# Kernel optimization log

Hardware: AMD Instinct MI355X
Metric: run time of the kernel (lower is better)

## Reference

```python
import jax, jax.numpy as jnp
import numpy as np

EMB, HEADS = 1024, 16
HS = EMB // HEADS
LN_EPS = 1e-5


def _layernorm(v, g, b):
    # normalize over last dim (headsize)
    mu = jnp.mean(v, axis=-1, keepdims=True)
    var = jnp.mean(jnp.square(v - mu), axis=-1, keepdims=True)
    return (v - mu) * jax.lax.rsqrt(var + LN_EPS) * g + b


def setup_inputs() -> dict:
    key = jax.random.key(0)
    ks = jax.random.split(key, 12)
    s = 1.0 / np.sqrt(EMB)
    return {
        "x": jax.random.normal(ks[0], (4, 2048, EMB), dtype=jnp.float32),
        "mask": jax.random.randint(ks[1], (4, 2048), 0, 2, dtype=jnp.int32),
        "Wk": jax.random.uniform(ks[2], (EMB, EMB), jnp.float32, -s, s),
        "Wq": jax.random.uniform(ks[3], (EMB, EMB), jnp.float32, -s, s),
        "Wv": jax.random.uniform(ks[4], (EMB, EMB), jnp.float32, -s, s),
        "Wo": jax.random.uniform(ks[5], (EMB, EMB), jnp.float32, -s, s),
        "bo": jax.random.uniform(ks[6], (EMB,), jnp.float32, -s, s),
        "kln_g": jnp.ones((HS,), jnp.float32),
        "kln_b": jnp.zeros((HS,), jnp.float32),
        "qln_g": jnp.ones((HS,), jnp.float32),
        "qln_b": jnp.zeros((HS,), jnp.float32),
    }


def reference(x, mask, Wk, Wq, Wv, Wo, bo, kln_g, kln_b, qln_g, qln_b):
    b, t, e = x.shape
    # QKV projections (torch Linear: y = x @ W.T), split into heads
    k = (x @ Wk.T).reshape(b, t, HEADS, HS)
    q = (x @ Wq.T).reshape(b, t, HEADS, HS)
    v = (x @ Wv.T).reshape(b, t, HEADS, HS)
    # per-head LayerNorm on K and Q
    k = _layernorm(k, kln_g, kln_b)
    q = _layernorm(q, qln_g, qln_b)
    # scale by emb^(1/4) on each side
    scale = jnp.asarray(e, x.dtype) ** 0.25
    q = q / scale
    k = k / scale
    # [b, h, tq, tk] attention logits
    dot = jnp.einsum("bqhd,bkhd->bhqk", q, k)
    # outer-product mask, broadcast over heads
    m = mask.astype(x.dtype)
    dm = m[:, None, :, None] * m[:, None, None, :]  # [b,1,tq,tk]
    # non-memory-efficient masked softmax: softmax(v*m)*m renormalized
    attn = jax.nn.softmax(dot * dm, axis=-1) * dm
    attn = attn / (jnp.sum(attn, axis=-1, keepdims=True) + 1e-13)
    out = jnp.einsum("bhqk,bkhd->bqhd", attn, v).reshape(b, t, e)
    return out @ Wo.T + bo
```

## Files before the change

kernel.cpp:

```cpp
#include <hip/hip_runtime.h>
#include <math.h>

#define B_SZ   4
#define T_SEQ  2048
#define EMB    1024
#define HEADS  16
#define HS     64
#define M_TOT  (B_SZ * T_SEQ)

typedef unsigned short u16;
using f32x4  = __attribute__((ext_vector_type(4))) float;
using bf16x8 = __attribute__((ext_vector_type(8))) short;
using u16x8  = __attribute__((ext_vector_type(8))) unsigned short;
using u16x4  = __attribute__((ext_vector_type(4))) unsigned short;

__device__ __forceinline__ void async16(u16* lds, const u16* g) {
    __builtin_amdgcn_global_load_lds(
        (const __attribute__((address_space(1))) unsigned int*)g,
        (__attribute__((address_space(3))) unsigned int*)lds, 16, 0, 0);
}

__device__ __forceinline__ u16 bf16_rne(float f) {
    unsigned u = __float_as_uint(f);
    return (u16)((u + 0x7fffu + ((u >> 16) & 1u)) >> 16);
}
__device__ __forceinline__ void split2(float f, u16& h, u16& l) {
    h = bf16_rne(f);
    float hf = __uint_as_float(((unsigned)h) << 16);
    l = bf16_rne(f - hf);
}
__device__ __forceinline__ unsigned cvt_pk_bf16(float a, float b) {
    unsigned r;
    asm("v_cvt_pk_bf16_f32 %0, %1, %2" : "=v"(r) : "v"(a), "v"(b));
    return r;
}

__global__ __launch_bounds__(256) void split_bf16(
    const float* __restrict__ in, u16* __restrict__ hi,
    u16* __restrict__ lo, int n4)
{
    int i = blockIdx.x * blockDim.x + threadIdx.x;
    if (i >= n4) return;
    float4 v = ((const float4*)in)[i];
    float f[4] = {v.x, v.y, v.z, v.w};
    u16 hh[4], ll[4];
    #pragma unroll
    for (int j = 0; j < 4; ++j) split2(f[j], hh[j], ll[j]);
    uint2 H, L;
    H.x = (unsigned)hh[0] | ((unsigned)hh[1] << 16);
    H.y = (unsigned)hh[2] | ((unsigned)hh[3] << 16);
    L.x = (unsigned)ll[0] | ((unsigned)ll[1] << 16);
    L.y = (unsigned)ll[2] | ((unsigned)ll[3] << 16);
    ((uint2*)hi)[i] = H;
    ((uint2*)lo)[i] = L;
}

#define BM 128
#define BN 128
#define BKB 32

__global__ __launch_bounds__(256, 2) void gemm_mfma(
    const u16* __restrict__ Ah, const u16* __restrict__ Al,
    const u16* __restrict__ Wh, const u16* __restrict__ Wl,
    float* __restrict__ Cf, u16* __restrict__ Chi, u16* __restrict__ Clo,
    const float* __restrict__ lng, const float* __restrict__ lnb,
    float post_scale, const float* __restrict__ bias, int mode)
{
    __shared__ u16 sAh[BM * BKB], sAl[BM * BKB];
    __shared__ u16 sBh[BN * BKB], sBl[BN * BKB];
    const int tid = threadIdx.x;
    const int w = tid >> 6, lane = tid & 63;
    const int wr = w >> 1, wc = w & 1;
    const int m0 = blockIdx.x * BM, n0 = blockIdx.y * BN;
    const int fr = lane & 15, kc = (lane >> 4) * 8;
    const int srow = lane >> 2, schunk = (lane & 3) * 8;

    f32x4 acc[4][4] = {};

    for (int k0 = 0; k0 < EMB; k0 += BKB) {
        #pragma unroll
        for (int c = 0; c < 2; ++c) {
            int r = (w * 2 + c) * 16 + srow;
            size_t gA = (size_t)(m0 + r) * EMB + k0 + schunk;
            size_t gB = (size_t)(n0 + r) * EMB + k0 + schunk;
            int lb = (w * 2 + c) * 512;
            async16(&sAh[lb], Ah + gA);
            async16(&sAl[lb], Al + gA);
            async16(&sBh[lb], Wh + gB);
            async16(&sBl[lb], Wl + gB);
        }
        __syncthreads();

        bf16x8 bh[4], bl[4];
        #pragma unroll
        for (int ni = 0; ni < 4; ++ni) {
            int row = wc * 64 + ni * 16 + fr;
            bh[ni] = *(const bf16x8*)&sBh[row * BKB + kc];
            bl[ni] = *(const bf16x8*)&sBl[row * BKB + kc];
        }
        #pragma unroll
        for (int mi = 0; mi < 4; ++mi) {
            int row = wr * 64 + mi * 16 + fr;
            bf16x8 ah = *(const bf16x8*)&sAh[row * BKB + kc];
            bf16x8 al = *(const bf16x8*)&sAl[row * BKB + kc];
            #pragma unroll
            for (int ni = 0; ni < 4; ++ni) {
                acc[mi][ni] = __builtin_amdgcn_mfma_f32_16x16x32_bf16(ah, bh[ni], acc[mi][ni], 0, 0, 0);
                acc[mi][ni] = __builtin_amdgcn_mfma_f32_16x16x32_bf16(ah, bl[ni], acc[mi][ni], 0, 0, 0);
                acc[mi][ni] = __builtin_amdgcn_mfma_f32_16x16x32_bf16(al, bh[ni], acc[mi][ni], 0, 0, 0);
            }
        }
        __syncthreads();
    }

    if (mode == 1) {
        float g4[4], b4[4];
        #pragma unroll
        for (int ni = 0; ni < 4; ++ni) {
            int dd = ni * 16 + fr;
            g4[ni] = lng[dd];
            b4[ni] = lnb[dd];
        }
        #pragma unroll
        for (int mi = 0; mi < 4; ++mi) {
            #pragma unroll
            for (int i = 0; i < 4; ++i) {
                float s = acc[mi][0][i] + acc[mi][1][i] + acc[mi][2][i] + acc[mi][3][i];
                #pragma unroll
                for (int off = 1; off < 16; off <<= 1) s += __shfl_xor(s, off);
                float mu = s * (1.f / HS);
                float d2 = 0.f;
                #pragma unroll
                for (int ni = 0; ni < 4; ++ni) {
                    float d = acc[mi][ni][i] - mu;
                    d2 += d * d;
                }
                #pragma unroll
                for (int off = 1; off < 16; off <<= 1) d2 += __shfl_xor(d2, off);
                float rs = rsqrtf(d2 * (1.f / HS) + 1e-5f);
                #pragma unroll
                for (int ni = 0; ni < 4; ++ni)
                    acc[mi][ni][i] = ((acc[mi][ni][i] - mu) * rs * g4[ni] + b4[ni]) * post_scale;
            }
        }
    }

    #pragma unroll
    for (int mi = 0; mi < 4; ++mi) {
        #pragma unroll
        for (int ni = 0; ni < 4; ++ni) {
            const int col = n0 + wc * 64 + ni * 16 + fr;
            const int rowb = m0 + wr * 64 + mi * 16 + (lane >> 4) * 4;
            if (mode == 0) {
                float badd = bias[col];
                #pragma unroll
                for (int i = 0; i < 4; ++i)
                    Cf[(size_t)(rowb + i) * EMB + col] = acc[mi][ni][i] + badd;
            } else if (mode == 1) {
                #pragma unroll
                for (int i = 0; i < 4; ++i) {
                    u16 hh, ll; split2(acc[mi][ni][i], hh, ll);
                    Chi[(size_t)(rowb + i) * EMB + col] = hh;
                    Clo[(size_t)(rowb + i) * EMB + col] = ll;
                }
            } else {
                int hh = col >> 6, d = col & 63;
                int bb = rowb >> 11, t0 = rowb & 2047;
                u16x4 H, L;
                #pragma unroll
                for (int i = 0; i < 4; ++i) {
                    u16 vh, vl; split2(acc[mi][ni][i], vh, vl);
                    H[i] = vh; L[i] = vl;
                }
                size_t off = ((size_t)((bb * HEADS + hh) * HS + d)) * T_SEQ + t0;
                *(u16x4*)(Chi + off) = H;
                *(u16x4*)(Clo + off) = L;
            }
        }
    }
}

__global__ __launch_bounds__(256, 2) void attn_mfma(
    const u16* __restrict__ qh, const u16* __restrict__ ql,
    const u16* __restrict__ kh, const u16* __restrict__ kl,
    const u16* __restrict__ vh, const u16* __restrict__ vl,
    const int* __restrict__ mask,
    u16* __restrict__ oh, u16* __restrict__ ol)
{
    __shared__ u16 sKh[64 * 72], sKl[64 * 72], sVh[64 * 72], sVl[64 * 72];
    __shared__ u16 sPs[4][32 * 72];
    __shared__ float kmsh[64];
    __shared__ float qmsh[128];
    __shared__ float fb[4][32];

    const int tid = threadIdx.x;
    const int w = tid >> 6, lane = tid & 63;
    const int fr = lane & 15, g = lane >> 4;
    const int q0 = blockIdx.x * 128;
    const int h = blockIdx.y, b = blockIdx.z;

    if (tid < 128) qmsh[tid] = (float)mask[b * T_SEQ + q0 + tid];

    const u16* ksrc; u16* sdst; size_t rstr, kstp;
    if (w < 2) {
        ksrc = (w == 0 ? kh : kl) + (size_t)b * T_SEQ * EMB + h * HS;
        sdst = (w == 0 ? sKh : sKl);
        rstr = EMB; kstp = (size_t)64 * EMB;
    } else {
        ksrc = (w == 2 ? vh : vl) + (size_t)(b * HEADS + h) * HS * T_SEQ;
        sdst = (w == 2 ? sVh : sVl);
        rstr = T_SEQ; kstp = 64;
    }

    bf16x8 qfh[2][2], qfl[2][2];
    #pragma unroll
    for (int nf = 0; nf < 2; ++nf)
        #pragma unroll
        for (int ks = 0; ks < 2; ++ks) {
            size_t off = (size_t)(b * T_SEQ + q0 + w * 32 + nf * 16 + fr) * EMB
                         + h * HS + g * 8 + ks * 32;
            qfh[nf][ks] = *(const bf16x8*)(qh + off);
            qfl[nf][ks] = *(const bf16x8*)(ql + off);
        }

    f32x4 o[2][4] = {};
    float mrun[2] = {-INFINITY, -INFINITY}, lrun[2] = {0.f, 0.f};
    u16* Psw = sPs[w];

    for (int kt = 0; kt < T_SEQ / 64; ++kt) {
        const u16* src = ksrc + (size_t)kt * kstp;
        u16x8 stg[8];
        #pragma unroll
        for (int it = 0; it < 8; ++it) {
            int idx = it * 64 + lane;
            stg[it] = *(const u16x8*)(src + (size_t)(idx >> 3) * rstr + (idx & 7) * 8);
        }
        #pragma unroll
        for (int it = 0; it < 8; ++it) {
            int idx = it * 64 + lane;
            *(u16x8*)&sdst[(idx >> 3) * 72 + (idx & 7) * 8] = stg[it];
        }
        if (tid < 64) kmsh[tid] = (float)mask[b * T_SEQ + kt * 64 + tid];
        __syncthreads();

        float kmv[4][4]; int anyv = 0;
        #pragma unroll
        for (int mf = 0; mf < 4; ++mf)
            #pragma unroll
            for (int i = 0; i < 4; ++i) {
                kmv[mf][i] = kmsh[mf * 16 + g * 4 + i];
                anyv |= (kmv[mf][i] != 0.f);
            }

        if (__any(anyv)) {
            f32x4 st[4][2] = {};
            #pragma unroll
            for (int ks = 0; ks < 2; ++ks) {
                bf16x8 ka[4], kb[4];
                #pragma unroll
                for (int mf = 0; mf < 4; ++mf) {
                    ka[mf] = *(const bf16x8*)&sKh[(mf * 16 + fr) * 72 + g * 8 + ks * 32];
                    kb[mf] = *(const bf16x8*)&sKl[(mf * 16 + fr) * 72 + g * 8 + ks * 32];
                }
                #pragma unroll
                for (int mf = 0; mf < 4; ++mf)
                    #pragma unroll
                    for (int nf = 0; nf < 2; ++nf) {
                        st[mf][nf] = __builtin_amdgcn_mfma_f32_16x16x32_bf16(ka[mf], qfh[nf][ks], st[mf][nf], 0, 0, 0);
                        st[mf][nf] = __builtin_amdgcn_mfma_f32_16x16x32_bf16(ka[mf], qfl[nf][ks], st[mf][nf], 0, 0, 0);
                        st[mf][nf] = __builtin_amdgcn_mfma_f32_16x16x32_bf16(kb[mf], qfh[nf][ks], st[mf][nf], 0, 0, 0);
                    }
            }
            #pragma unroll
            for (int nf = 0; nf < 2; ++nf) {
                float tm = -INFINITY;
                #pragma unroll
                for (int mf = 0; mf < 4; ++mf)
                    #pragma unroll
                    for (int i = 0; i < 4; ++i) {
                        float s = (kmv[mf][i] != 0.f) ? st[mf][nf][i] : -INFINITY;
                        st[mf][nf][i] = s;
                        tm = fmaxf(tm, s);
                    }
                tm = fmaxf(tm, __shfl_xor(tm, 16));
                tm = fmaxf(tm, __shfl_xor(tm, 32));
                float mn = fmaxf(mrun[nf], tm);
                float f = __expf(mrun[nf] - mn);
                float ps = 0.f;
                #pragma unroll
                for (int mf = 0; mf < 4; ++mf)
                    #pragma unroll
                    for (int i = 0; i < 4; ++i) {
                        float p = __expf(st[mf][nf][i] - mn);
                        st[mf][nf][i] = p;
                        ps += p;
                    }
                ps += __shfl_xor(ps, 16);
                ps += __shfl_xor(ps, 32);
                lrun[nf] = lrun[nf] * f + ps;
                mrun[nf] = mn;
                fb[w][nf * 16 + fr] = f;
            }
            #pragma unroll
            for (int nf = 0; nf < 2; ++nf)
                #pragma unroll
                for (int mf = 0; mf < 4; ++mf)
                    #pragma unroll
                    for (int i = 0; i < 4; i += 2) {
                        unsigned pk = cvt_pk_bf16(st[mf][nf][i], st[mf][nf][i + 1]);
                        *(unsigned*)&Psw[(nf * 16 + fr) * 72 + mf * 16 + g * 4 + i] = pk;
                    }
            float ff[2][4];
            #pragma unroll
            for (int mi = 0; mi < 2; ++mi)
                #pragma unroll
                for (int i = 0; i < 4; ++i)
                    ff[mi][i] = fb[w][mi * 16 + g * 4 + i];
            #pragma unroll
            for (int mi = 0; mi < 2; ++mi)
                #pragma unroll
                for (int nj = 0; nj < 4; ++nj)
                    #pragma unroll
                    for (int i = 0; i < 4; ++i)
                        o[mi][nj][i] *= ff[mi][i];
            #pragma unroll
            for (int ks = 0; ks < 2; ++ks) {
                bf16x8 pa[2];
                #pragma unroll
                for (int mi = 0; mi < 2; ++mi)
                    pa[mi] = *(const bf16x8*)&Psw[(mi * 16 + fr) * 72 + g * 8 + ks * 32];
                #pragma unroll
                for (int nj = 0; nj < 4; ++nj) {
                    bf16x8 va = *(const bf16x8*)&sVh[(nj * 16 + fr) * 72 + g * 8 + ks * 32];
                    bf16x8 vb = *(const bf16x8*)&sVl[(nj * 16 + fr) * 72 + g * 8 + ks * 32];
                    #pragma unroll
                    for (int mi = 0; mi < 2; ++mi) {
                        o[mi][nj] = __builtin_amdgcn_mfma_f32_16x16x32_bf16(pa[mi], va, o[mi][nj], 0, 0, 0);
                        o[mi][nj] = __builtin_amdgcn_mfma_f32_16x16x32_bf16(pa[mi], vb, o[mi][nj], 0, 0, 0);
                    }
                }
            }
        }
        __syncthreads();
    }

    #pragma unroll
    for (int nf = 0; nf < 2; ++nf) fb[w][nf * 16 + fr] = lrun[nf];
    #pragma unroll
    for (int mi = 0; mi < 2; ++mi)
        #pragma unroll
        for (int i = 0; i < 4; ++i) {
            float lq = fb[w][mi * 16 + g * 4 + i];
            float qv = qmsh[w * 32 + mi * 16 + g * 4 + i];
            float inv = (qv != 0.f && lq > 0.f) ? 1.f / lq : 0.f;
            size_t row = (size_t)(b * T_SEQ + q0 + w * 32 + mi * 16 + g * 4 + i);
            #pragma unroll
            for (int nj = 0; nj < 4; ++nj) {
                float v = o[mi][nj][i] * inv;
                u16 hh, ll; split2(v, hh, ll);
                size_t off = row * EMB + h * HS + nj * 16 + fr;
                oh[off] = hh;
                ol[off] = ll;
            }
        }
}

extern "C" void kernel_launch(void* const* d_in, const int* in_sizes, int n_in,
                              void* d_out, int out_size, void* d_ws, size_t ws_size,
                              hipStream_t stream)
{
    const float* x    = (const float*)d_in[0];
    const int*   mask = (const int*)d_in[1];
    const float* Wk   = (const float*)d_in[2];
    const float* Wq   = (const float*)d_in[3];
    const float* Wv   = (const float*)d_in[4];
    const float* Wo   = (const float*)d_in[5];
    const float* bo   = (const float*)d_in[6];
    const float* kg   = (const float*)d_in[7];
    const float* kbb  = (const float*)d_in[8];
    const float* qg   = (const float*)d_in[9];
    const float* qbb  = (const float*)d_in[10];
    float* out = (float*)d_out;

    const size_t NELT = (size_t)M_TOT * EMB;
    const size_t WELT = (size_t)EMB * EMB;
    u16* xh  = (u16*)d_ws;
    u16* xl  = xh + NELT;
    u16* p_qh = xl + NELT;
    u16* p_ql = p_qh + NELT;
    u16* p_kh = p_ql + NELT;
    u16* p_kl = p_kh + NELT;
    u16* p_vh = p_kl + NELT;
    u16* p_vl = p_vh + NELT;
    u16* wqh = p_vl + NELT;
    u16* wql = wqh + WELT;
    u16* wkh = wql + WELT;
    u16* wkl = wkh + WELT;
    u16* wvh = wkl + WELT;
    u16* wvl = wvh + WELT;
    u16* woh = wvl + WELT;
    u16* wol = woh + WELT;

    const float ps = 0.17677669529663687f;

    split_bf16<<<(int)(NELT / 4 + 255) / 256, 256, 0, stream>>>(x, xh, xl, (int)(NELT / 4));
    split_bf16<<<(int)(WELT / 4 + 255) / 256, 256, 0, stream>>>(Wq, wqh, wql, (int)(WELT / 4));
    split_bf16<<<(int)(WELT / 4 + 255) / 256, 256, 0, stream>>>(Wk, wkh, wkl, (int)(WELT / 4));
    split_bf16<<<(int)(WELT / 4 + 255) / 256, 256, 0, stream>>>(Wv, wvh, wvl, (int)(WELT / 4));
    split_bf16<<<(int)(WELT / 4 + 255) / 256, 256, 0, stream>>>(Wo, woh, wol, (int)(WELT / 4));

    dim3 ggrid(M_TOT / BM, EMB / BN);
    gemm_mfma<<<ggrid, 256, 0, stream>>>(xh, xl, wqh, wql, nullptr, p_qh, p_ql, qg, qbb, ps, nullptr, 1);
    gemm_mfma<<<ggrid, 256, 0, stream>>>(xh, xl, wkh, wkl, nullptr, p_kh, p_kl, kg, kbb, ps, nullptr, 1);
    gemm_mfma<<<ggrid, 256, 0, stream>>>(xh, xl, wvh, wvl, nullptr, p_vh, p_vl, nullptr, nullptr, 1.f, nullptr, 2);

    dim3 agrid(T_SEQ / 128, HEADS, B_SZ);
    attn_mfma<<<agrid, 256, 0, stream>>>(p_qh, p_ql, p_kh, p_kl, p_vh, p_vl, mask, xh, xl);

    gemm_mfma<<<ggrid, 256, 0, stream>>>(xh, xl, woh, wol, out, nullptr, nullptr, nullptr, nullptr, 1.f, bo, 0);
}
```

Baseline: 550.7 us.

## Widen attention blocks to 256 queries, fuse split kernels, add MFMA priority

The attention kernel now uses 512-thread blocks that each cover 256 query rows. Each K/V tile loaded into LDS is therefore shared by eight waves instead of four, and every wave stages only half a tile. The five fp32→bf16 hi/lo split launches are merged into one kernel that picks its source by index range. s_setprio is raised around the MFMA sections, and a guard skips the exp work when a row's running max is still -inf. The __launch_bounds__(512,4) hint caps registers tightly and could cause spills. LDS use per block roughly doubles, which may limit how many blocks fit on a CU.

```diff
diff --git a/kernel.cpp b/kernel.cpp
--- a/kernel.cpp
+++ b/kernel.cpp
@@ -35,13 +35,25 @@
     return r;
 }
 
-__global__ __launch_bounds__(256) void split_bf16(
-    const float* __restrict__ in, u16* __restrict__ hi,
-    u16* __restrict__ lo, int n4)
+__global__ __launch_bounds__(256) void split_all(
+    const float* __restrict__ x,  const float* __restrict__ wq,
+    const float* __restrict__ wk, const float* __restrict__ wv,
+    const float* __restrict__ wo,
+    u16* __restrict__ xh,  u16* __restrict__ xl,
+    u16* __restrict__ wqh, u16* __restrict__ wql,
+    u16* __restrict__ wkh, u16* __restrict__ wkl,
+    u16* __restrict__ wvh, u16* __restrict__ wvl,
+    u16* __restrict__ woh, u16* __restrict__ wol)
 {
-    int i = blockIdx.x * blockDim.x + threadIdx.x;
-    if (i >= n4) return;
-    float4 v = ((const float4*)in)[i];
+    int i = blockIdx.x * 256 + threadIdx.x;
+    int r = i >> 18;
+    const float* src; u16* dh; u16* dl; int off;
+    if (r < 8)       { src = x;  dh = xh;  dl = xl;  off = i; }
+    else if (r == 8) { src = wq; dh = wqh; dl = wql; off = i - (8 << 18); }
+    else if (r == 9) { src = wk; dh = wkh; dl = wkl; off = i - (9 << 18); }
+    else if (r == 10){ src = wv; dh = wvh; dl = wvl; off = i - (10 << 18); }
+    else             { src = wo; dh = woh; dl = wol; off = i - (11 << 18); }
+    float4 v = ((const float4*)src)[off];
     float f[4] = {v.x, v.y, v.z, v.w};
     u16 hh[4], ll[4];
     #pragma unroll
@@ -51,8 +63,8 @@
     H.y = (unsigned)hh[2] | ((unsigned)hh[3] << 16);
     L.x = (unsigned)ll[0] | ((unsigned)ll[1] << 16);
     L.y = (unsigned)ll[2] | ((unsigned)ll[3] << 16);
-    ((uint2*)hi)[i] = H;
-    ((uint2*)lo)[i] = L;
+    ((uint2*)dh)[off] = H;
+    ((uint2*)dl)[off] = L;
 }
 
 #define BM 128
@@ -180,7 +192,7 @@
     }
 }
 
-__global__ __launch_bounds__(256, 2) void attn_mfma(
+__global__ __launch_bounds__(512, 4) void attn_mfma(
     const u16* __restrict__ qh, const u16* __restrict__ ql,
     const u16* __restrict__ kh, const u16* __restrict__ kl,
     const u16* __restrict__ vh, const u16* __restrict__ vl,
@@ -188,29 +200,27 @@
     u16* __restrict__ oh, u16* __restrict__ ol)
 {
     __shared__ u16 sKh[64 * 72], sKl[64 * 72], sVh[64 * 72], sVl[64 * 72];
-    __shared__ u16 sPs[4][32 * 72];
+    __shared__ u16 sPs[8][32 * 72];
     __shared__ float kmsh[64];
-    __shared__ float qmsh[128];
-    __shared__ float fb[4][32];
+    __shared__ float qmsh[256];
+    __shared__ float fb[8][32];
 
     const int tid = threadIdx.x;
     const int w = tid >> 6, lane = tid & 63;
     const int fr = lane & 15, g = lane >> 4;
-    const int q0 = blockIdx.x * 128;
+    const int q0 = blockIdx.x * 256;
     const int h = blockIdx.y, b = blockIdx.z;
 
-    if (tid < 128) qmsh[tid] = (float)mask[b * T_SEQ + q0 + tid];
-
-    const u16* ksrc; u16* sdst; size_t rstr, kstp;
-    if (w < 2) {
-        ksrc = (w == 0 ? kh : kl) + (size_t)b * T_SEQ * EMB + h * HS;
-        sdst = (w == 0 ? sKh : sKl);
-        rstr = EMB; kstp = (size_t)64 * EMB;
-    } else {
-        ksrc = (w == 2 ? vh : vl) + (size_t)(b * HEADS + h) * HS * T_SEQ;
-        sdst = (w == 2 ? sVh : sVl);
-        rstr = T_SEQ; kstp = 64;
-    }
+    if (tid < 256) qmsh[tid] = (float)mask[b * T_SEQ + q0 + tid];
+
+    const int bsel = w >> 1, half = w & 1;
+    const u16* gsrc; u16* sdst; int rstr; size_t kstep;
+    if (bsel == 0)      { gsrc = kh + (size_t)b * T_SEQ * EMB + h * HS; sdst = sKh; rstr = EMB;   kstep = (size_t)64 * EMB; }
+    else if (bsel == 1) { gsrc = kl + (size_t)b * T_SEQ * EMB + h * HS; sdst = sKl; rstr = EMB;   kstep = (size_t)64 * EMB; }
+    else if (bsel == 2) { gsrc = vh + (size_t)(b * HEADS + h) * HS * T_SEQ; sdst = sVh; rstr = T_SEQ; kstep = 64; }
+    else                { gsrc = vl + (size_t)(b * HEADS + h) * HS * T_SEQ; sdst = sVl; rstr = T_SEQ; kstep = 64; }
+    gsrc += (size_t)half * 32 * rstr;
+    sdst += half * 32 * 72;
 
     bf16x8 qfh[2][2], qfl[2][2];
     #pragma unroll
@@ -228,15 +238,15 @@
     u16* Psw = sPs[w];
 
     for (int kt = 0; kt < T_SEQ / 64; ++kt) {
-        const u16* src = ksrc + (size_t)kt * kstp;
-        u16x8 stg[8];
-        #pragma unroll
-        for (int it = 0; it < 8; ++it) {
+        const u16* src = gsrc + (size_t)kt * kstep;
+        u16x8 stg[4];
+        #pragma unroll
+        for (int it = 0; it < 4; ++it) {
             int idx = it * 64 + lane;
             stg[it] = *(const u16x8*)(src + (size_t)(idx >> 3) * rstr + (idx & 7) * 8);
         }
         #pragma unroll
-        for (int it = 0; it < 8; ++it) {
+        for (int it = 0; it < 4; ++it) {
             int idx = it * 64 + lane;
             *(u16x8*)&sdst[(idx >> 3) * 72 + (idx & 7) * 8] = stg[it];
         }
@@ -262,6 +272,7 @@
                     ka[mf] = *(const bf16x8*)&sKh[(mf * 16 + fr) * 72 + g * 8 + ks * 32];
                     kb[mf] = *(const bf16x8*)&sKl[(mf * 16 + fr) * 72 + g * 8 + ks * 32];
                 }
+                __builtin_amdgcn_s_setprio(1);
                 #pragma unroll
                 for (int mf = 0; mf < 4; ++mf)
                     #pragma unroll
@@ -270,6 +281,7 @@
                         st[mf][nf] = __builtin_amdgcn_mfma_f32_16x16x32_bf16(ka[mf], qfl[nf][ks], st[mf][nf], 0, 0, 0);
                         st[mf][nf] = __builtin_amdgcn_mfma_f32_16x16x32_bf16(kb[mf], qfh[nf][ks], st[mf][nf], 0, 0, 0);
                     }
+                __builtin_amdgcn_s_setprio(0);
             }
             #pragma unroll
             for (int nf = 0; nf < 2; ++nf) {
@@ -285,21 +297,29 @@
                 tm = fmaxf(tm, __shfl_xor(tm, 16));
                 tm = fmaxf(tm, __shfl_xor(tm, 32));
                 float mn = fmaxf(mrun[nf], tm);
-                float f = __expf(mrun[nf] - mn);
-                float ps = 0.f;
-                #pragma unroll
-                for (int mf = 0; mf < 4; ++mf)
-                    #pragma unroll
-                    for (int i = 0; i < 4; ++i) {
-                        float p = __expf(st[mf][nf][i] - mn);
-                        st[mf][nf][i] = p;
-                        ps += p;
-                    }
-                ps += __shfl_xor(ps, 16);
-                ps += __shfl_xor(ps, 32);
-                lrun[nf] = lrun[nf] * f + ps;
-                mrun[nf] = mn;
-                fb[w][nf * 16 + fr] = f;
+                if (mn != -INFINITY) {
+                    float f = __expf(mrun[nf] - mn);
+                    float ps = 0.f;
+                    #pragma unroll
+                    for (int mf = 0; mf < 4; ++mf)
+                        #pragma unroll
+                        for (int i = 0; i < 4; ++i) {
+                            float p = __expf(st[mf][nf][i] - mn);
+                            st[mf][nf][i] = p;
+                            ps += p;
+                        }
+                    ps += __shfl_xor(ps, 16);
+                    ps += __shfl_xor(ps, 32);
+                    lrun[nf] = lrun[nf] * f + ps;
+                    mrun[nf] = mn;
+                    fb[w][nf * 16 + fr] = f;
+                } else {
+                    #pragma unroll
+                    for (int mf = 0; mf < 4; ++mf)
+                        #pragma unroll
+                        for (int i = 0; i < 4; ++i) st[mf][nf][i] = 0.f;
+                    fb[w][nf * 16 + fr] = 1.f;
+                }
             }
             #pragma unroll
             for (int nf = 0; nf < 2; ++nf)
@@ -329,6 +349,7 @@
                 #pragma unroll
                 for (int mi = 0; mi < 2; ++mi)
                     pa[mi] = *(const bf16x8*)&Psw[(mi * 16 + fr) * 72 + g * 8 + ks * 32];
+                __builtin_amdgcn_s_setprio(1);
                 #pragma unroll
                 for (int nj = 0; nj < 4; ++nj) {
                     bf16x8 va = *(const bf16x8*)&sVh[(nj * 16 + fr) * 72 + g * 8 + ks * 32];
@@ -339,6 +360,7 @@
                         o[mi][nj] = __builtin_amdgcn_mfma_f32_16x16x32_bf16(pa[mi], vb, o[mi][nj], 0, 0, 0);
                     }
                 }
+                __builtin_amdgcn_s_setprio(0);
             }
         }
         __syncthreads();
@@ -347,7 +369,7 @@
     #pragma unroll
     for (int nf = 0; nf < 2; ++nf) fb[w][nf * 16 + fr] = lrun[nf];
     #pragma unroll
-    for (int mi = 0; mi < 2; ++mi)
+    for (int mi = 0; mi < 2; ++mi) {
         #pragma unroll
         for (int i = 0; i < 4; ++i) {
             float lq = fb[w][mi * 16 + g * 4 + i];
@@ -363,6 +385,7 @@
                 ol[off] = ll;
             }
         }
+    }
 }
 
 extern "C" void kernel_launch(void* const* d_in, const int* in_sizes, int n_in,
@@ -403,19 +426,16 @@
 
     const float ps = 0.17677669529663687f;
 
-    split_bf16<<<(int)(NELT / 4 + 255) / 256, 256, 0, stream>>>(x, xh, xl, (int)(NELT / 4));
-    split_bf16<<<(int)(WELT / 4 + 255) / 256, 256, 0, stream>>>(Wq, wqh, wql, (int)(WELT / 4));
-    split_bf16<<<(int)(WELT / 4 + 255) / 256, 256, 0, stream>>>(Wk, wkh, wkl, (int)(WELT / 4));
-    split_bf16<<<(int)(WELT / 4 + 255) / 256, 256, 0, stream>>>(Wv, wvh, wvl, (int)(WELT / 4));
-    split_bf16<<<(int)(WELT / 4 + 255) / 256, 256, 0, stream>>>(Wo, woh, wol, (int)(WELT / 4));
+    split_all<<<12288, 256, 0, stream>>>(x, Wq, Wk, Wv, Wo,
+        xh, xl, wqh, wql, wkh, wkl, wvh, wvl, woh, wol);
 
     dim3 ggrid(M_TOT / BM, EMB / BN);
     gemm_mfma<<<ggrid, 256, 0, stream>>>(xh, xl, wqh, wql, nullptr, p_qh, p_ql, qg, qbb, ps, nullptr, 1);
     gemm_mfma<<<ggrid, 256, 0, stream>>>(xh, xl, wkh, wkl, nullptr, p_kh, p_kl, kg, kbb, ps, nullptr, 1);
     gemm_mfma<<<ggrid, 256, 0, stream>>>(xh, xl, wvh, wvl, nullptr, p_vh, p_vl, nullptr, nullptr, 1.f, nullptr, 2);
 
-    dim3 agrid(T_SEQ / 128, HEADS, B_SZ);
-    attn_mfma<<<agrid, 256, 0, stream>>>(p_qh, p_ql, p_kh, p_kl, p_vh, p_vl, mask, xh, xl);
+    dim3 agrid(T_SEQ / 256, HEADS, B_SZ);
+    attn_mfma<<<agrid, 512, 0, stream>>>(p_qh, p_ql, p_kh, p_kl, p_vh, p_vl, mask, xh, xl);
 
     gemm_mfma<<<ggrid, 256, 0, stream>>>(xh, xl, woh, wol, out, nullptr, nullptr, nullptr, nullptr, 1.f, bo, 0);
 }
```

New measurement: 0.9997 ms. 1.82x slower.
